# Kernel optimization log

Hardware: AMD Instinct MI355X
Metric: run time of the kernel (lower is better)

Reference implementation:

```python
import jax, jax.numpy as jnp
import numpy as np

B, T, K = 16, 1024, 1024
LEAK = 0.1
LN2PI = 1.8378770664093453  # log(2*pi)


def setup_inputs() -> dict:
    key = jax.random.key(0)
    k1, k2 = jax.random.split(key)
    obvs = jax.random.normal(k1, (B, T), dtype=jnp.float32)
    mu = jax.random.normal(k2, (K,), dtype=jnp.float32)
    ln_sigma = jnp.zeros((K,), dtype=jnp.float32)
    # CategoricalPrior: uniform log-prior
    ln_pi = jnp.full((K,), -np.log(float(K)), dtype=jnp.float32)
    # LeakyTransfer(K, 0.1): A = (1-eps)*I + eps/K
    A = (1.0 - LEAK) * np.eye(K, dtype=np.float64) + LEAK / K
    ln_A = jnp.asarray(np.log(A), dtype=jnp.float32)
    return {"obvs": obvs, "mu": mu, "ln_sigma": ln_sigma, "ln_pi": ln_pi, "ln_A": ln_A}


def reference(obvs, mu, ln_sigma, ln_pi, ln_A):
    # Gaussian emission log-probs: [B, T, K]
    diff = obvs[:, :, None] - mu  # [B,T,K]
    ln_e = -0.5 * diff * diff * jnp.exp(-2.0 * ln_sigma) - ln_sigma - 0.5 * LN2PI
    ln_e_t = jnp.swapaxes(ln_e, 0, 1)  # [T, B, K]

    def transfer(x):  # log-space matvec: out[b,j] = lse_i(x[b,i] + ln_A[i,j])
        return jax.nn.logsumexp(x[:, :, None] + ln_A[None, :, :], axis=1)

    # forward recurrence: f_0 = e_0 + ln_pi ; f_t = e_t + transfer(f_{t-1})
    f0 = ln_e_t[0] + ln_pi
    def fstep(c, e):
        n = e + transfer(c)
        return n, n
    _, fs = jax.lax.scan(fstep, f0, ln_e_t[1:])
    ln_fs = jnp.concatenate([f0[None], fs], axis=0)  # [T,B,K]

    # backward recurrence (faithful to source): b_{T-1} = ln_pi (prior on zeros);
    # b_t = transfer(b_{t+1} + e_{t+1})
    bT = jnp.broadcast_to(ln_pi, (B, K)).astype(ln_e.dtype)
    def bstep(c, e):
        n = transfer(c + e)
        return n, n
    _, bs = jax.lax.scan(bstep, bT, ln_e_t[1:], reverse=True)  # bs[t] = b_t for t in [0, T-2]
    ln_bs = jnp.concatenate([bs, bT[None]], axis=0)  # [T,B,K]

    ln_gamma = ln_fs + ln_bs
    res = ln_gamma - jax.nn.logsumexp(ln_gamma, axis=2, keepdims=True)
    return jnp.swapaxes(res, 0, 1)  # [B, T, K]
```

## Files before the change

### kernel.cpp

```cpp
#include <hip/hip_runtime.h>
#include <cstdint>

constexpr int B_ = 16, T_ = 1024, K_ = 1024;
constexpr int L2_ = 16;
constexpr int H_  = L2_ / 2;
constexpr int W2_ = 24;
constexpr int NF_ = T_ / L2_;
constexpr int SON_ = W2_ + L2_ + W2_ + 1;
constexpr float LOG2E_ = 1.4426950408889634f;
constexpr float LN2_   = 0.6931471805599453f;

typedef float f32x2 __attribute__((ext_vector_type(2)));

template <int CTRL>
__device__ __forceinline__ float dpp_add(float v) {
  int t = __builtin_amdgcn_update_dpp(0, __builtin_bit_cast(int, v), CTRL, 0xF, 0xF, true);
  return v + __builtin_bit_cast(float, t);
}
__device__ __forceinline__ float wave_sum64_dpp(float v) {
  v = dpp_add<0x111>(v);
  v = dpp_add<0x112>(v);
  v = dpp_add<0x114>(v);
  v = dpp_add<0x118>(v);
  v = dpp_add<0x142>(v);
  v = dpp_add<0x143>(v);
  return __builtin_bit_cast(float, __builtin_amdgcn_readlane(__builtin_bit_cast(int, v), 63));
}

__device__ __forceinline__ float red8_dpp(const f32x2 v[8]) {
  const f32x2 w0 = v[0] + v[1], w1 = v[2] + v[3], w2 = v[4] + v[5], w3 = v[6] + v[7];
  const f32x2 u0 = w0 + w1, u1 = w2 + w3;
  const f32x2 z = u0 + u1;
  return wave_sum64_dpp(z[0] + z[1]);
}

__device__ __forceinline__ uint32_t cvt_pk_bf16(float lo, float hi) {
  uint32_t r;
  asm("v_cvt_pk_bf16_f32 %0, %1, %2" : "=v"(r) : "v"(lo), "v"(hi));
  return r;
}

extern "C" __global__ void __launch_bounds__(128, 2)
hmm_fusedA(const float* __restrict__ obvs, const float* __restrict__ mu,
           const float* __restrict__ ln_sigma, const float* __restrict__ ln_pi,
           const float* __restrict__ ln_A, float* __restrict__ outp) {
  __shared__ float so[SON_];
  __shared__ alignas(16) uint16_t aL[H_ * K_];
  __shared__ alignas(16) uint16_t bL[H_ * K_];

  const int tid  = threadIdx.x;
  const int lane = tid & 63;
  const int wid  = tid >> 6;
  const int c = blockIdx.x & (NF_ - 1);
  const int b = blockIdx.x >> 6;
  const int t0 = c * L2_, t1 = t0 + L2_;
  const int base = t0 - W2_;

  for (int i = tid; i < SON_; i += 128) {
    const int t = base + i;
    if (t >= 0 && t < T_) so[i] = obvs[b * T_ + t];
  }
  __syncthreads();

  const float offd = __expf(ln_A[1]);
  const float dmo  = __expf(ln_A[0]) - offd;
  const float ds   = dmo / offd;
  const float lof  = __builtin_amdgcn_logf(offd);
  f32x2 c2v[8], c1v[8], c0v[8];
#pragma unroll
  for (int q = 0; q < 4; ++q) {
    const float4 m  = reinterpret_cast<const float4*>(mu)[q * 64 + lane];
    const float4 ls = reinterpret_cast<const float4*>(ln_sigma)[q * 64 + lane];
    const float mm[4] = {m.x, m.y, m.z, m.w};
    const float ll[4] = {ls.x, ls.y, ls.z, ls.w};
#pragma unroll
    for (int e = 0; e < 4; ++e) {
      const float niv = -0.5f * __builtin_amdgcn_exp2f(-2.0f * ll[e] * LOG2E_) * LOG2E_;
      c2v[2*q + e/2][e%2] = niv;
      c1v[2*q + e/2][e%2] = -2.0f * niv * mm[e];
      c0v[2*q + e/2][e%2] = __builtin_fmaf(niv * mm[e], mm[e], lof - ll[e] * LOG2E_);
    }
  }
  const f32x2 one2 = {1.0f, 1.0f};
  const f32x2 ln2_2 = {LN2_, LN2_};

#define EMIS_O(OV, H)                                                          \
  {                                                                            \
    const f32x2 o2_ = {(OV), (OV)};                                            \
    _Pragma("unroll")                                                          \
    for (int i = 0; i < 8; ++i) {                                              \
      const f32x2 t_ = o2_ * c2v[i] + c1v[i];                                  \
      const f32x2 a_ = o2_ * t_ + c0v[i];                                      \
      (H)[i][0] = __builtin_amdgcn_exp2f(a_[0]);                               \
      (H)[i][1] = __builtin_amdgcn_exp2f(a_[1]);                               \
    }                                                                          \
  }
#define EMIS(T_IDX, H) { const float oE_ = so[(T_IDX) - base]; EMIS_O(oE_, H) }

#define STORE_ROW(BASEP, R, X)                                                 \
  {                                                                            \
    uint2* pw_ = reinterpret_cast<uint2*>((BASEP) + (R) * K_);                 \
    _Pragma("unroll")                                                          \
    for (int q = 0; q < 4; ++q) {                                              \
      uint2 w_;                                                                \
      w_.x = cvt_pk_bf16((X)[2*q][0], (X)[2*q][1]);                            \
      w_.y = cvt_pk_bf16((X)[2*q+1][0], (X)[2*q+1][1]);                        \
      pw_[q * 64 + lane] = w_;                                                 \
    }                                                                          \
  }

#define GAMMA_ROW(LROW, T_ABS, XR)                                             \
  {                                                                            \
    f32x2 p_[8];                                                               \
    const uint2* pr_ = reinterpret_cast<const uint2*>(LROW);                   \
    _Pragma("unroll")                                                          \
    for (int q = 0; q < 4; ++q) {                                              \
      const uint2 w_ = pr_[q * 64 + lane];                                     \
      f32x2 a0_, a1_;                                                          \
      a0_[0] = __builtin_bit_cast(float, w_.x << 16);                          \
      a0_[1] = __builtin_bit_cast(float, w_.x & 0xFFFF0000u);                  \
      a1_[0] = __builtin_bit_cast(float, w_.y << 16);                          \
      a1_[1] = __builtin_bit_cast(float, w_.y & 0xFFFF0000u);                  \
      p_[2*q]   = a0_ * (XR)[2*q];                                             \
      p_[2*q+1] = a1_ * (XR)[2*q+1];                                           \
    }                                                                          \
    const float S_ = red8_dpp(p_);                                             \
    const float nls_ = -__builtin_amdgcn_logf(S_) * LN2_;                      \
    const f32x2 nl2_ = {nls_, nls_};                                           \
    float4* op_ = reinterpret_cast<float4*>(outp + ((size_t)b * T_ + (T_ABS)) * K_);\
    _Pragma("unroll")                                                          \
    for (int q = 0; q < 4; ++q) {                                              \
      f32x2 l0_, l1_;                                                          \
      l0_[0] = __builtin_amdgcn_logf(p_[2*q][0]);                              \
      l0_[1] = __builtin_amdgcn_logf(p_[2*q][1]);                              \
      l1_[0] = __builtin_amdgcn_logf(p_[2*q+1][0]);                            \
      l1_[1] = __builtin_amdgcn_logf(p_[2*q+1][1]);                            \
      l0_ = l0_ * ln2_2 + nl2_;                                                \
      l1_ = l1_ * ln2_2 + nl2_;                                                \
      float4 ov_ = {l0_[0], l0_[1], l1_[0], l1_[1]};                           \
      op_[q * 64 + lane] = ov_;                                                \
    }                                                                          \
  }

#define FWD_STEP_P(HNEXT_T)                                                    \
  {                                                                            \
    f32x2 hN_[8];                                                              \
    EMIS(HNEXT_T, hN_);                                                        \
    const float sf_ = ds * __builtin_amdgcn_rcpf(red8_dpp(x));                 \
    const f32x2 s2_ = {sf_, sf_};                                              \
    _Pragma("unroll")                                                          \
    for (int i = 0; i < 8; ++i) x[i] = h[i] * (s2_ * x[i] + one2);             \
    _Pragma("unroll")                                                          \
    for (int i = 0; i < 8; ++i) h[i] = hN_[i];                                 \
  }

#define BWD_STEP_P(HNEXT_T)                                                    \
  {                                                                            \
    f32x2 hN_[8];                                                              \
    EMIS(HNEXT_T, hN_);                                                        \
    f32x2 ub_[8];                                                              \
    _Pragma("unroll")                                                          \
    for (int i = 0; i < 8; ++i) ub_[i] = h[i] * x[i];                          \
    const float sb_ = ds * __builtin_amdgcn_rcpf(red8_dpp(ub_));               \
    const f32x2 s2_ = {sb_, sb_};                                              \
    _Pragma("unroll")                                                          \
    for (int i = 0; i < 8; ++i) x[i] = s2_ * ub_[i] + one2;                    \
    _Pragma("unroll")                                                          \
    for (int i = 0; i < 8; ++i) h[i] = hN_[i];                                 \
  }

  f32x2 x[8], h[8];

  if (wid == 0) {
    int bstart, nburn, jst = 0;
    if (t0 - W2_ <= 0) {
      f32x2 h0[8];
      EMIS(0, h0);
#pragma unroll
      for (int q = 0; q < 4; ++q) {
        const float4 p4 = reinterpret_cast<const float4*>(ln_pi)[q * 64 + lane];
        x[2*q][0]   = __expf(p4.x) * h0[2*q][0];
        x[2*q][1]   = __expf(p4.y) * h0[2*q][1];
        x[2*q+1][0] = __expf(p4.z) * h0[2*q+1][0];
        x[2*q+1][1] = __expf(p4.w) * h0[2*q+1][1];
      }
      if (t0 == 0) { STORE_ROW(aL, 0, x); jst = 1; }
      bstart = 1;
      nburn = (t0 > 0) ? (t0 - 1) : 0;
    } else {
#pragma unroll
      for (int i = 0; i < 8; ++i) x[i] = one2;
      bstart = t0 - W2_ + 1;
      nburn = W2_ - 1;
    }
    EMIS(bstart, h);
#pragma unroll 2
    for (int i = 0; i < nburn; ++i) {
      FWD_STEP_P(bstart + i + 1)
    }
#pragma unroll 1
    for (int j = jst; j < H_; ++j) {
      FWD_STEP_P(t0 + j + 1)
      STORE_ROW(aL, j, x);
    }
  } else {
    int btB, nburnB, jhi = L2_ - 1;
    if (t1 - 1 + W2_ >= T_ - 1) {
#pragma unroll
      for (int q = 0; q < 4; ++q) {
        const float4 p4 = reinterpret_cast<const float4*>(ln_pi)[q * 64 + lane];
        x[2*q][0] = __expf(p4.x);   x[2*q][1] = __expf(p4.y);
        x[2*q+1][0] = __expf(p4.z); x[2*q+1][1] = __expf(p4.w);
      }
      if (t1 == T_) { STORE_ROW(bL, L2_ - 1 - H_, x); jhi = L2_ - 2; }
      btB = T_ - 2;
      nburnB = (T_ - 1) - t1;
      if (nburnB < 0) nburnB = 0;
    } else {
#pragma unroll
      for (int i = 0; i < 8; ++i) x[i] = one2;
      btB = t1 + W2_ - 2;
      nburnB = W2_ - 1;
    }
    EMIS(btB + 1, h);
#pragma unroll 2
    for (int i = 0; i < nburnB; ++i) {
      BWD_STEP_P(btB - i)
    }
#pragma unroll 1
    for (int j = jhi; j >= H_; --j) {
      BWD_STEP_P(t0 + j)
      STORE_ROW(bL, j - H_, x);
    }
  }

  __syncthreads();

  if (wid == 0) {
#pragma unroll 1
    for (int j = H_; j < L2_; ++j) {
      FWD_STEP_P(t0 + j + 1)
      GAMMA_ROW(bL + (j - H_) * K_, t0 + j, x);
    }
  } else {
#pragma unroll 1
    for (int j = H_ - 1; j >= 0; --j) {
      BWD_STEP_P(t0 + j)
      GAMMA_ROW(aL + j * K_, t0 + j, x);
    }
  }
#undef EMIS
#undef EMIS_O
#undef STORE_ROW
#undef GAMMA_ROW
#undef FWD_STEP_P
#undef BWD_STEP_P
}

extern "C" void kernel_launch(void* const* d_in, const int* in_sizes, int n_in,
                              void* d_out, int out_size, void* d_ws, size_t ws_size,
                              hipStream_t stream) {
  const float* obvs     = (const float*)d_in[0];
  const float* mu       = (const float*)d_in[1];
  const float* ln_sigma = (const float*)d_in[2];
  const float* ln_pi    = (const float*)d_in[3];
  const float* ln_A     = (const float*)d_in[4];
  float* out = (float*)d_out;
  (void)d_ws; (void)ws_size;

  hipLaunchKernelGGL(hmm_fusedA, dim3(B_ * NF_), dim3(128), 0, stream,
                     obvs, mu, ln_sigma, ln_pi, ln_A, out);
}
```

Before: 28.64 us.

## Halve time-chunk length, double block count, drop emission prefetch pipelining

The time chunk per block shrinks from 16 to 8 steps, so twice as many blocks run, and launch bounds now target 4 blocks per CU. The emission software pipeline (precomputing the next step's emission into a second register array) is removed to cut register pressure, and the burn-in loops are no longer unrolled. The aim is more parallelism and occupancy to hide the serial recurrence latency. The cost is that the 24-step burn-in warmup is now amortised over only 8 output steps, so total recurrence work rises sharply, and emission latency is no longer hidden.

```diff
diff --git a/kernel.cpp b/kernel.cpp
--- a/kernel.cpp
+++ b/kernel.cpp
@@ -2,7 +2,7 @@
 #include <cstdint>
 
 constexpr int B_ = 16, T_ = 1024, K_ = 1024;
-constexpr int L2_ = 16;
+constexpr int L2_ = 8;
 constexpr int H_  = L2_ / 2;
 constexpr int W2_ = 24;
 constexpr int NF_ = T_ / L2_;
@@ -40,8 +40,8 @@
   return r;
 }
 
-extern "C" __global__ void __launch_bounds__(128, 2)
-hmm_fusedA(const float* __restrict__ obvs, const float* __restrict__ mu,
+extern "C" __global__ void __launch_bounds__(128, 4)
+hmm_fusedB(const float* __restrict__ obvs, const float* __restrict__ mu,
            const float* __restrict__ ln_sigma, const float* __restrict__ ln_pi,
            const float* __restrict__ ln_A, float* __restrict__ outp) {
   __shared__ float so[SON_];
@@ -52,7 +52,7 @@
   const int lane = tid & 63;
   const int wid  = tid >> 6;
   const int c = blockIdx.x & (NF_ - 1);
-  const int b = blockIdx.x >> 6;
+  const int b = blockIdx.x >> 7;
   const int t0 = c * L2_, t1 = t0 + L2_;
   const int base = t0 - W2_;
 
@@ -142,34 +142,29 @@
     }                                                                          \
   }
 
-#define FWD_STEP_P(HNEXT_T)                                                    \
-  {                                                                            \
-    f32x2 hN_[8];                                                              \
-    EMIS(HNEXT_T, hN_);                                                        \
+#define FWD_STEP(T_IDX)                                                        \
+  {                                                                            \
+    f32x2 hf_[8];                                                              \
+    EMIS(T_IDX, hf_);                                                          \
     const float sf_ = ds * __builtin_amdgcn_rcpf(red8_dpp(x));                 \
     const f32x2 s2_ = {sf_, sf_};                                              \
     _Pragma("unroll")                                                          \
-    for (int i = 0; i < 8; ++i) x[i] = h[i] * (s2_ * x[i] + one2);             \
-    _Pragma("unroll")                                                          \
-    for (int i = 0; i < 8; ++i) h[i] = hN_[i];                                 \
-  }
-
-#define BWD_STEP_P(HNEXT_T)                                                    \
-  {                                                                            \
-    f32x2 hN_[8];                                                              \
-    EMIS(HNEXT_T, hN_);                                                        \
-    f32x2 ub_[8];                                                              \
-    _Pragma("unroll")                                                          \
-    for (int i = 0; i < 8; ++i) ub_[i] = h[i] * x[i];                          \
+    for (int i = 0; i < 8; ++i) x[i] = hf_[i] * (s2_ * x[i] + one2);           \
+  }
+
+#define BWD_STEP(T_IDX)                                                        \
+  {                                                                            \
+    f32x2 hb_[8], ub_[8];                                                      \
+    EMIS((T_IDX) + 1, hb_);                                                    \
+    _Pragma("unroll")                                                          \
+    for (int i = 0; i < 8; ++i) ub_[i] = hb_[i] * x[i];                        \
     const float sb_ = ds * __builtin_amdgcn_rcpf(red8_dpp(ub_));               \
     const f32x2 s2_ = {sb_, sb_};                                              \
     _Pragma("unroll")                                                          \
     for (int i = 0; i < 8; ++i) x[i] = s2_ * ub_[i] + one2;                    \
-    _Pragma("unroll")                                                          \
-    for (int i = 0; i < 8; ++i) h[i] = hN_[i];                                 \
-  }
-
-  f32x2 x[8], h[8];
+  }
+
+  f32x2 x[8];
 
   if (wid == 0) {
     int bstart, nburn, jst = 0;
@@ -193,14 +188,13 @@
       bstart = t0 - W2_ + 1;
       nburn = W2_ - 1;
     }
-    EMIS(bstart, h);
-#pragma unroll 2
+#pragma unroll 1
     for (int i = 0; i < nburn; ++i) {
-      FWD_STEP_P(bstart + i + 1)
+      FWD_STEP(bstart + i)
     }
 #pragma unroll 1
     for (int j = jst; j < H_; ++j) {
-      FWD_STEP_P(t0 + j + 1)
+      FWD_STEP(t0 + j)
       STORE_ROW(aL, j, x);
     }
   } else {
@@ -222,14 +216,13 @@
       btB = t1 + W2_ - 2;
       nburnB = W2_ - 1;
     }
-    EMIS(btB + 1, h);
-#pragma unroll 2
+#pragma unroll 1
     for (int i = 0; i < nburnB; ++i) {
-      BWD_STEP_P(btB - i)
+      BWD_STEP(btB - i)
     }
 #pragma unroll 1
     for (int j = jhi; j >= H_; --j) {
-      BWD_STEP_P(t0 + j)
+      BWD_STEP(t0 + j)
       STORE_ROW(bL, j - H_, x);
     }
   }
@@ -239,13 +232,13 @@
   if (wid == 0) {
 #pragma unroll 1
     for (int j = H_; j < L2_; ++j) {
-      FWD_STEP_P(t0 + j + 1)
+      FWD_STEP(t0 + j)
       GAMMA_ROW(bL + (j - H_) * K_, t0 + j, x);
     }
   } else {
 #pragma unroll 1
     for (int j = H_ - 1; j >= 0; --j) {
-      BWD_STEP_P(t0 + j)
+      BWD_STEP(t0 + j)
       GAMMA_ROW(aL + j * K_, t0 + j, x);
     }
   }
@@ -253,8 +246,8 @@
 #undef EMIS_O
 #undef STORE_ROW
 #undef GAMMA_ROW
-#undef FWD_STEP_P
-#undef BWD_STEP_P
+#undef FWD_STEP
+#undef BWD_STEP
 }
 
 extern "C" void kernel_launch(void* const* d_in, const int* in_sizes, int n_in,
@@ -268,6 +261,6 @@
   float* out = (float*)d_out;
   (void)d_ws; (void)ws_size;
 
-  hipLaunchKernelGGL(hmm_fusedA, dim3(B_ * NF_), dim3(128), 0, stream,
+  hipLaunchKernelGGL(hmm_fusedB, dim3(B_ * NF_), dim3(128), 0, stream,
                      obvs, mu, ln_sigma, ln_pi, ln_A, out);
 }
```

Measured after the change: 33.20 us. 15.9% more time.
